# Performance work log

Hardware: AMD Instinct MI355X
Metric: run time of the kernel (lower is better)

## Reference

```python
import jax, jax.numpy as jnp
import numpy as np

K = 5       # kernel_size
UP = 2      # up_factor
EPS = 1e-5  # BatchNorm eps (eval mode)


def _conv(x, w, pad, dil=1):
    return jax.lax.conv_general_dilated(
        x, w, (1, 1), [(pad, pad), (pad, pad)], rhs_dilation=(dil, dil),
        dimension_numbers=('NCHW', 'OIHW', 'NCHW'))


def _bn(x, g, b, m, v):
    inv = g / jnp.sqrt(v + EPS)
    return x * inv[:, None, None] + (b - m * inv)[:, None, None]


def _bilinear(x, oh, ow):
    # torch F.interpolate(mode='bilinear', align_corners=False)
    N, C, H, W = x.shape
    def coords(out_s, in_s):
        s = in_s / out_s
        src = (jnp.arange(out_s, dtype=jnp.float32) + 0.5) * s - 0.5
        src = jnp.clip(src, 0.0, in_s - 1)
        i0 = jnp.floor(src).astype(jnp.int32)
        i1 = jnp.minimum(i0 + 1, in_s - 1)
        return i0, i1, src - i0
    y0, y1, wy = coords(oh, H)
    x0, x1, wx = coords(ow, W)
    g = lambda yi, xi: x[:, :, yi][:, :, :, xi]  # (N,C,oh,ow)
    top = g(y0, x0) * (1 - wx) + g(y0, x1) * wx
    bot = g(y1, x0) * (1 - wx) + g(y1, x1) * wx
    return top * (1 - wy)[:, None] + bot * wy[:, None]


def _unfold(x):
    # F.unfold(k=5, pad=2) reshaped to (N, C, K*K, H, W); channel-major (c, kh, kw)
    p = K // 2
    N, C, H, W = x.shape
    xp = jnp.pad(x, ((0, 0), (0, 0), (p, p), (p, p)))
    patches = [xp[:, :, i:i + H, j:j + W] for i in range(K) for j in range(K)]
    return jnp.stack(patches, axis=2)


def setup_inputs() -> dict:
    key = jax.random.key(0)
    ks = jax.random.split(key, 8)
    N, C, H, W = 2, 256, 48, 48
    Cc = C // 4
    Cout = 256
    d = {}
    d['x'] = jax.random.normal(ks[0], (N, C, H, W), dtype=jnp.float32)
    d['compress_w'] = jax.random.normal(ks[1], (Cc, C, 1, 1), dtype=jnp.float32) * 0.05
    d['g1'] = jnp.ones((Cc,), jnp.float32)
    d['b1'] = jnp.zeros((Cc,), jnp.float32)
    d['m1'] = jax.random.normal(ks[2], (Cc,), dtype=jnp.float32) * 0.1
    d['v1'] = jax.random.uniform(ks[3], (Cc,), minval=0.5, maxval=1.5, dtype=jnp.float32)
    d['ke1_w'] = jax.random.normal(ks[4], (Cc, Cc, 3, 3), dtype=jnp.float32) * 0.05
    d['gk'] = jnp.ones((Cc,), jnp.float32)
    d['bk'] = jnp.zeros((Cc,), jnp.float32)
    d['mk'] = jax.random.normal(ks[5], (Cc,), dtype=jnp.float32) * 0.1
    d['vk'] = jax.random.uniform(ks[6], (Cc,), minval=0.5, maxval=1.5, dtype=jnp.float32)
    d['ke2_w'] = jax.random.normal(ks[7], (UP * UP * K * K, Cc, 3, 3), dtype=jnp.float32) * 0.05
    d['proj_w'] = jax.random.normal(jax.random.fold_in(key, 10), (Cout, C, 1, 1), dtype=jnp.float32) * 0.05
    d['g2'] = jnp.ones((Cout,), jnp.float32)
    d['b2'] = jnp.zeros((Cout,), jnp.float32)
    d['m2'] = jax.random.normal(jax.random.fold_in(key, 11), (Cout,), dtype=jnp.float32) * 0.1
    d['v2'] = jax.random.uniform(jax.random.fold_in(key, 12), (Cout,), minval=0.5, maxval=1.5, dtype=jnp.float32)
    return d


def reference(x, compress_w, g1, b1, m1, v1, ke1_w, gk, bk, mk, vk, ke2_w,
              proj_w, g2, b2, m2, v2):
    N, C, H, W = x.shape
    oh, ow = H * UP, W * UP
    # kernel prediction branch
    comp = jax.nn.relu(_bn(_conv(x, compress_w, 0), g1, b1, m1, v1))
    k1 = jax.nn.relu(_bn(_conv(comp, ke1_w, 2, dil=2), gk, bk, mk, vk))
    kernel = _conv(k1, ke2_w, 1)                               # (N, UP^2*K^2, H, W)
    kernel = jax.nn.softmax(kernel.reshape(N, UP * UP, K * K, H, W), axis=2)
    # content reassembly
    x_up = jnp.repeat(jnp.repeat(x, UP, axis=2), UP, axis=3)
    x_unf = _unfold(x_up)                                      # (N, C, K^2, oh, ow)
    k_up = _bilinear(kernel.reshape(N, UP * UP * K * K, H, W), oh, ow)
    k_up = k_up.reshape(N, UP * UP, K * K, oh, ow)
    out = jnp.einsum('nckhw,nukhw->nuchw', x_unf, k_up)        # (N, UP^2, C, oh, ow)
    # view (N, UP^2*C, oh, ow) then pixel_shuffle(UP)
    out = out.reshape(N, UP * UP * C, oh, ow)
    out = out.reshape(N, C, UP, UP, oh, ow)
    out = out.transpose(0, 1, 4, 2, 5, 3).reshape(N, C, oh * UP, ow * UP)
    out = jax.nn.relu(_bn(_conv(out, proj_w, 0), g2, b2, m2, v2))
    return out
```

## Files before the change

### kernel.cpp

```cpp
#include <hip/hip_runtime.h>

#define EPSB 1e-5f

typedef __attribute__((ext_vector_type(8))) short bf16x8;
typedef __attribute__((ext_vector_type(4))) float f32x4;

__device__ __forceinline__ unsigned short f2b(float f) {
  union { float f; unsigned u; } cv; cv.f = f;
  unsigned r = cv.u + 0x7FFFu + ((cv.u >> 16) & 1u);
  return (unsigned short)(r >> 16);
}

__global__ __launch_bounds__(256) void k_prep(
    const float* __restrict__ pw, const float* __restrict__ cw,
    const float* __restrict__ k1w, const float* __restrict__ k2w,
    const float* __restrict__ g1, const float* __restrict__ b1,
    const float* __restrict__ m1, const float* __restrict__ v1,
    const float* __restrict__ gk, const float* __restrict__ bk,
    const float* __restrict__ mk, const float* __restrict__ vk,
    const float* __restrict__ g2, const float* __restrict__ b2,
    const float* __restrict__ m2, const float* __restrict__ v2,
    unsigned short* __restrict__ pwb, unsigned short* __restrict__ wcb_t,
    unsigned short* __restrict__ wt1, unsigned short* __restrict__ wt2,
    float* __restrict__ sb1, float* __restrict__ sbk, float* __restrict__ sb2,
    float* __restrict__ wsz) {
  int i = blockIdx.x * 256 + threadIdx.x;
  if (i < 333056) wsz[i] = 0.f;
  if (i < 65536) pwb[i] = f2b(pw[i]);
  int j = i - 65536;
  if (j >= 0 && j < 16384) { int ci = j >> 6, co = j & 63; wcb_t[j] = f2b(cw[co * 256 + ci]); }
  int a = i - 81920;
  if (a >= 0 && a < 36864) {
    int co = a / 576, k = a % 576, tap = k >> 6, ci = k & 63;
    wt1[a] = f2b(k1w[co * 576 + ci * 9 + tap]);
  }
  int c2 = i - 118784;
  if (c2 >= 0 && c2 < 73728) {
    int co = c2 / 576, k = c2 % 576, tap = k >> 6, ci = k & 63;
    wt2[c2] = (co < 100) ? f2b(k2w[co * 576 + ci * 9 + tap]) : (unsigned short)0;
  }
  int s = i - 192512;
  if (s >= 0 && s < 64) { float iv = g1[s] / sqrtf(v1[s] + EPSB); sb1[s] = iv; sb1[64 + s] = b1[s] - m1[s] * iv; }
  if (s >= 64 && s < 128) { int c = s - 64; float iv = gk[c] / sqrtf(vk[c] + EPSB); sbk[c] = iv; sbk[64 + c] = bk[c] - mk[c] * iv; }
  if (s >= 128 && s < 384) { int c = s - 128; float iv = g2[c] / sqrtf(v2[c] + EPSB); sb2[c] = iv; sb2[256 + c] = b2[c] - m2[c] * iv; }
}

__global__ __launch_bounds__(256) void k_compress(
    const float* __restrict__ x, const unsigned short* __restrict__ wcb_t,
    const float* __restrict__ sb1, unsigned short* __restrict__ comp_t) {
  __shared__ unsigned short wl[16384];
  int t = threadIdx.x;
  for (int f = t; f < 2048; f += 256)
    *(bf16x8*)&wl[f * 8] = *(const bf16x8*)&wcb_t[f * 8];
  __syncthreads();
  int idx = blockIdx.x * 256 + t;
  int co2 = (idx & 31) * 2;
  int pg = idx >> 5;
  int n = pg / 1152;
  int pix0 = (pg % 1152) * 2;
  const float* xp = x + (size_t)n * 256 * 2304 + pix0;
  float a00 = 0.f, a01 = 0.f, a10 = 0.f, a11 = 0.f;
  for (int ci = 0; ci < 256; ++ci) {
    float2 xv = *(const float2*)(xp + (size_t)ci * 2304);
    unsigned pr = *(const unsigned*)&wl[ci * 64 + co2];
    union { unsigned u; float f; } wa, wb;
    wa.u = pr << 16; wb.u = pr & 0xffff0000u;
    a00 = fmaf(xv.x, wa.f, a00); a01 = fmaf(xv.y, wa.f, a01);
    a10 = fmaf(xv.x, wb.f, a10); a11 = fmaf(xv.y, wb.f, a11);
  }
  float s0 = sb1[co2], s1 = sb1[co2 + 1];
  float c0b = sb1[64 + co2], c1b = sb1[64 + co2 + 1];
  float o00 = fmaxf(fmaf(a00, s0, c0b), 0.f), o01 = fmaxf(fmaf(a01, s0, c0b), 0.f);
  float o10 = fmaxf(fmaf(a10, s1, c1b), 0.f), o11 = fmaxf(fmaf(a11, s1, c1b), 0.f);
  int r = pix0 / 48, c = pix0 % 48;
  unsigned short* ob = comp_t + ((size_t)n * 2704 + (r + 2) * 52 + (c + 2)) * 64 + co2;
  unsigned p0 = (unsigned)f2b(o00) | ((unsigned)f2b(o10) << 16);
  unsigned p1 = (unsigned)f2b(o01) | ((unsigned)f2b(o11) << 16);
  *(unsigned*)&ob[0]  = p0;
  *(unsigned*)&ob[64] = p1;
}

__global__ __launch_bounds__(256) void k_ke1(
    const unsigned short* __restrict__ comp_t, const unsigned short* __restrict__ wt1,
    const float* __restrict__ sbk, unsigned short* __restrict__ k1_t) {
  __shared__ unsigned short sA[16640];
  int t = threadIdx.x;
  int bid = blockIdx.x;
  int n = bid / 48, y = bid % 48;
  const unsigned short* src = comp_t + ((size_t)n * 52 + y) * 52 * 64;
  for (int f = t; f < 2080; f += 256) {
    int g = f >> 3, ci0 = (f & 7) * 8;
    int cc = g % 52, rr = g / 52;
    bf16x8 vv = *(const bf16x8*)&src[(rr * 52 + cc) * 64 + ci0];
    int ba = (((rr * 52 + cc) * 64 + ci0) * 2) ^ ((cc & 7) << 4);
    *(bf16x8*)((char*)sA + ba) = vv;
  }
  __syncthreads();
  int wid = t >> 6, l = t & 63, l15 = l & 15, lg = l >> 4;
  f32x4 acc[3];
  acc[0] = acc[1] = acc[2] = (f32x4){0.f, 0.f, 0.f, 0.f};
  const unsigned short* arow = wt1 + (size_t)(wid * 16 + l15) * 576;
#pragma unroll
  for (int kbi = 0; kbi < 18; ++kbi) {
    int tap = kbi >> 1;
    int ky = tap / 3, kx = tap % 3;
    int ci0 = (kbi & 1) * 32 + lg * 8;
    bf16x8 afr = *(const bf16x8*)&arow[kbi * 32 + lg * 8];
#pragma unroll
    for (int nt = 0; nt < 3; ++nt) {
      int col = nt * 16 + l15 + 2 * kx;
      int ba = (((2 * ky * 52 + col) * 64 + ci0) * 2) ^ ((col & 7) << 4);
      bf16x8 bfr = *(const bf16x8*)((char*)sA + ba);
      acc[nt] = __builtin_amdgcn_mfma_f32_16x16x32_bf16(afr, bfr, acc[nt], 0, 0, 0);
    }
  }
  unsigned short* dst = k1_t + ((size_t)n * 50 + (y + 1)) * 50 * 64;
  int co0 = wid * 16 + lg * 4;
  float s0 = sbk[co0], s1 = sbk[co0 + 1], s2 = sbk[co0 + 2], s3 = sbk[co0 + 3];
  float d0 = sbk[64 + co0], d1 = sbk[64 + co0 + 1], d2 = sbk[64 + co0 + 2], d3 = sbk[64 + co0 + 3];
#pragma unroll
  for (int nt = 0; nt < 3; ++nt) {
    int px = nt * 16 + l15;
    ushort4 pk;
    pk.x = f2b(fmaxf(fmaf(acc[nt][0], s0, d0), 0.f));
    pk.y = f2b(fmaxf(fmaf(acc[nt][1], s1, d1), 0.f));
    pk.z = f2b(fmaxf(fmaf(acc[nt][2], s2, d2), 0.f));
    pk.w = f2b(fmaxf(fmaf(acc[nt][3], s3, d3), 0.f));
    *(ushort4*)&dst[(px + 1) * 64 + co0] = pk;
  }
}

__global__ __launch_bounds__(256) void k_ke2(
    const unsigned short* __restrict__ k1_t, const unsigned short* __restrict__ wt2,
    float* __restrict__ kern_t) {
  __shared__ unsigned short sA[9600];
  int t = threadIdx.x;
  int bid = blockIdx.x;
  int n = bid / 48, y = bid % 48;
  const unsigned short* src = k1_t + ((size_t)n * 50 + y) * 50 * 64;
  for (int f = t; f < 1200; f += 256) {
    int g = f >> 3, ci0 = (f & 7) * 8;
    int cc = g % 50, rr = g / 50;
    bf16x8 vv = *(const bf16x8*)&src[(rr * 50 + cc) * 64 + ci0];
    int ba = (((rr * 50 + cc) * 64 + ci0) * 2) ^ ((cc & 7) << 4);
    *(bf16x8*)((char*)sA + ba) = vv;
  }
  __syncthreads();
  int wid = t >> 6, l = t & 63, l15 = l & 15, lg = l >> 4;
  f32x4 acc[2][3];
#pragma unroll
  for (int mi = 0; mi < 2; ++mi)
#pragma unroll
    for (int nt = 0; nt < 3; ++nt) acc[mi][nt] = (f32x4){0.f, 0.f, 0.f, 0.f};
#pragma unroll
  for (int kbi = 0; kbi < 18; ++kbi) {
    int tap = kbi >> 1;
    int ky = tap / 3, kx = tap % 3;
    int ci0 = (kbi & 1) * 32 + lg * 8;
    bf16x8 afr[2];
#pragma unroll
    for (int mi = 0; mi < 2; ++mi)
      afr[mi] = *(const bf16x8*)&wt2[(size_t)((wid * 2 + mi) * 16 + l15) * 576 + kbi * 32 + lg * 8];
#pragma unroll
    for (int nt = 0; nt < 3; ++nt) {
      int col = nt * 16 + l15 + kx;
      int ba = (((ky * 50 + col) * 64 + ci0) * 2) ^ ((col & 7) << 4);
      bf16x8 bfr = *(const bf16x8*)((char*)sA + ba);
      acc[0][nt] = __builtin_amdgcn_mfma_f32_16x16x32_bf16(afr[0], bfr, acc[0][nt], 0, 0, 0);
      acc[1][nt] = __builtin_amdgcn_mfma_f32_16x16x32_bf16(afr[1], bfr, acc[1][nt], 0, 0, 0);
    }
  }
#pragma unroll
  for (int mi = 0; mi < 2; ++mi) {
    int co0 = (wid * 2 + mi) * 16 + lg * 4;
    if (co0 < 100) {
#pragma unroll
      for (int nt = 0; nt < 3; ++nt) {
        int px = nt * 16 + l15;
        float4 vv = {acc[mi][nt][0], acc[mi][nt][1], acc[mi][nt][2], acc[mi][nt][3]};
        *(float4*)&kern_t[((size_t)n * 2304 + y * 48 + px) * 112 + co0] = vv;
      }
    }
  }
}

__global__ __launch_bounds__(256) void k_w9sm(const float* __restrict__ kern_t,
                                              float* __restrict__ w9) {
  __shared__ float ks[3 * 48 * 116];
  int bid = blockIdx.x;
  int n = bid / 48, k = bid % 48;
  int t = threadIdx.x;
  int rows[3] = {max(k - 1, 0), k, min(k + 1, 47)};
#pragma unroll
  for (int s = 0; s < 3; ++s) {
    const float* src = kern_t + ((size_t)n * 2304 + rows[s] * 48) * 112;
    for (int f = t; f < 1344; f += 256) {
      float4 vv = *(const float4*)&src[f * 4];
      int sx = f / 28, c = (f % 28) * 4;
      *(float4*)&ks[(s * 48 + sx) * 116 + c] = vv;
    }
  }
  __syncthreads();
#pragma unroll
  for (int it = 0; it < 3; ++it) {
    int f = t + it * 256;
    int half = f / 384, rem = f % 384;
    int w2 = rem >> 2, u = rem & 3;
    int y96 = 2 * k + half;
    float syf = fminf(fmaxf(y96 * 0.5f - 0.25f, 0.f), 47.f);
    int y0 = (int)syf; int y1 = min(y0 + 1, 47); float wy = syf - (float)y0;
    int sl0 = (y0 == k) ? 1 : 0;
    int sl1 = (y1 == k) ? 1 : 2;
    float sxf = fminf(fmaxf(w2 * 0.5f - 0.25f, 0.f), 47.f);
    int x0 = (int)sxf; int x1 = min(x0 + 1, 47); float wx = sxf - (float)x0;
    float bl[25];
#pragma unroll
    for (int kk = 0; kk < 25; ++kk) bl[kk] = 0.f;
    float ws4[4] = {(1.f - wx) * (1.f - wy), wx * (1.f - wy), (1.f - wx) * wy, wx * wy};
    int ssy[4] = {sl0, sl0, sl1, sl1};
    int ssx[4] = {x0, x1, x0, x1};
#pragma unroll
    for (int s = 0; s < 4; ++s) {
      const float* p = &ks[(ssy[s] * 48 + ssx[s]) * 116 + u * 25];
      float vv[25], mx = -3.4e38f;
#pragma unroll
      for (int kk = 0; kk < 25; ++kk) { vv[kk] = p[kk]; mx = fmaxf(mx, vv[kk]); }
      float sum = 0.f;
#pragma unroll
      for (int kk = 0; kk < 25; ++kk) { vv[kk] = __expf(vv[kk] - mx); sum += vv[kk]; }
      float rs = ws4[s] / sum;
#pragma unroll
      for (int kk = 0; kk < 25; ++kk) bl[kk] = fmaf(vv[kk], rs, bl[kk]);
    }
#pragma unroll
    for (int kh = 0; kh < 5; ++kh) {
      bool vy = (unsigned)(y96 + kh - 2) < 96u;
#pragma unroll
      for (int kw = 0; kw < 5; ++kw) {
        bool vx = (unsigned)(w2 + kw - 2) < 96u;
        if (!(vy && vx)) bl[kh * 5 + kw] = 0.f;
      }
    }
    int py = y96 & 1, px_ = w2 & 1;
    float cc0[5], cc1[5], cc2[5];
#pragma unroll
    for (int kh = 0; kh < 5; ++kh) {
      cc0[kh] = px_ ? bl[kh * 5 + 0] : bl[kh * 5 + 0] + bl[kh * 5 + 1];
      cc1[kh] = px_ ? bl[kh * 5 + 1] + bl[kh * 5 + 2] : bl[kh * 5 + 2] + bl[kh * 5 + 3];
      cc2[kh] = px_ ? bl[kh * 5 + 3] + bl[kh * 5 + 4] : bl[kh * 5 + 4];
    }
    float* op = w9 + (((size_t)(n * 96 + y96) * 96 + w2) * 4 + u) * 9;
    op[0] = py ? cc0[0] : cc0[0] + cc0[1];
    op[1] = py ? cc1[0] : cc1[0] + cc1[1];
    op[2] = py ? cc2[0] : cc2[0] + cc2[1];
    op[3] = py ? cc0[1] + cc0[2] : cc0[2] + cc0[3];
    op[4] = py ? cc1[1] + cc1[2] : cc1[2] + cc1[3];
    op[5] = py ? cc2[1] + cc2[2] : cc2[2] + cc2[3];
    op[6] = py ? cc0[3] + cc0[4] : cc0[4];
    op[7] = py ? cc1[3] + cc1[4] : cc1[4];
    op[8] = py ? cc2[3] + cc2[4] : cc2[4];
  }
}

__global__ __launch_bounds__(512, 4) void k_reassemble_proj(
    const float* __restrict__ x, const float* __restrict__ w9,
    const unsigned short* __restrict__ pwb, const float* __restrict__ sb2,
    float* __restrict__ out) {
  __shared__ float xls[256 * 35];
  __shared__ float w9s[1152];
  __shared__ float sb2s[512];
  __shared__ unsigned short finT[64 * 256];

  int blk = blockIdx.x;
  int n = blk / 288;
  int r = blk % 288;
  int y48 = r / 6;
  int xt = r % 6;
  int X0 = xt * 32;
  int x480 = xt * 8;
  int t = threadIdx.x;

  sb2s[t] = sb2[t];
  {
    const float* base = w9 + ((size_t)(n * 96 + 2 * y48) * 96 + xt * 16) * 36;
    for (int f = t; f < 1152; f += 512) {
      int half = f / 576, o = f - half * 576;
      w9s[f] = base[(size_t)half * 3456 + o];
    }
  }
  const float* xb = x + (size_t)n * 256 * 2304;
  for (int f = t; f < 8448; f += 512) {
    int c = f / 33, rc = f - c * 33;
    int ry = rc / 11, cx = rc - ry * 11;
    int sy = min(max(y48 + ry - 1, 0), 47);
    int sx = min(max(x480 + cx - 1, 0), 47);
    int slot = (c & 3) * 64 + (c >> 2);
    xls[slot * 35 + rc] = xb[(size_t)c * 2304 + sy * 48 + sx];
  }
  __syncthreads();

  int ci = t & 255, rY = t >> 8;
  int u = ci >> 6, ch = ci & 63;
  int cb = ci >> 3, crr = ci & 7;
  int wid = t >> 6, l = t & 63, l15 = l & 15, lg = l >> 4;
  const unsigned short* a0p = pwb + (size_t)(wid * 2 * 16 + l15) * 256;
  const unsigned short* a1p = a0p + 16 * 256;
  size_t outn = (size_t)n * 256 * 36864;
  int Ybase = 4 * y48;

#pragma unroll
  for (int chunk = 0; chunk < 2; ++chunk) {
    {
      const float* xc0 = &xls[((rY * 2 + 0) * 64 + ch) * 35];
      const float* xc1 = &xls[((rY * 2 + 1) * 64 + ch) * 35];
      float xw0[9], xw1[9];
#pragma unroll
      for (int ry = 0; ry < 3; ++ry)
#pragma unroll
        for (int cx = 0; cx < 3; ++cx) {
          xw0[ry * 3 + cx] = xc0[ry * 11 + cx];
          xw1[ry * 3 + cx] = xc1[ry * 11 + cx];
        }
#pragma unroll
      for (int j = 0; j < 16; ++j) {
        if (j >= 2 && (j & 1) == 0) {
          int nc = (j >> 1) + 2;
#pragma unroll
          for (int ry = 0; ry < 3; ++ry) {
            xw0[ry*3+0]=xw0[ry*3+1]; xw0[ry*3+1]=xw0[ry*3+2]; xw0[ry*3+2]=xc0[ry*11+nc];
            xw1[ry*3+0]=xw1[ry*3+1]; xw1[ry*3+1]=xw1[ry*3+2]; xw1[ry*3+2]=xc1[ry*11+nc];
          }
        }
        const float* wt = &w9s[(chunk * 16 + j) * 36 + u * 9];
        float a0 = 0.f, a1 = 0.f;
#pragma unroll
        for (int k9 = 0; k9 < 9; ++k9) {
          float wv = wt[k9];
          a0 = fmaf(xw0[k9], wv, a0);
          a1 = fmaf(xw1[k9], wv, a1);
        }
        int px0 = rY * 32 + 2 * j, px1 = px0 + 1;
        finT[px0 * 256 + ((cb ^ (px0 & 7)) * 8 + crr)] = f2b(a0);
        finT[px1 * 256 + ((cb ^ (px1 & 7)) * 8 + crr)] = f2b(a1);
      }
    }
    __syncthreads();

    f32x4 acc[2][4];
#pragma unroll
    for (int mi = 0; mi < 2; ++mi)
#pragma unroll
      for (int nt = 0; nt < 4; ++nt) acc[mi][nt] = (f32x4){0.f, 0.f, 0.f, 0.f};
#pragma unroll
    for (int kbi = 0; kbi < 8; ++kbi) {
      bf16x8 afr0 = *(const bf16x8*)&a0p[kbi * 32 + lg * 8];
      bf16x8 afr1 = *(const bf16x8*)&a1p[kbi * 32 + lg * 8];
      int cbk = kbi * 4 + lg;
#pragma unroll
      for (int nt = 0; nt < 4; ++nt) {
        int row = nt * 16 + l15;
        bf16x8 bfr = *(const bf16x8*)&finT[row * 256 + ((cbk ^ (row & 7)) * 8)];
        acc[0][nt] = __builtin_amdgcn_mfma_f32_16x16x32_bf16(afr0, bfr, acc[0][nt], 0, 0, 0);
        acc[1][nt] = __builtin_amdgcn_mfma_f32_16x16x32_bf16(afr1, bfr, acc[1][nt], 0, 0, 0);
      }
    }
#pragma unroll
    for (int mi = 0; mi < 2; ++mi) {
      int mt = wid * 2 + mi;
#pragma unroll
      for (int r4 = 0; r4 < 4; ++r4) {
        int o = mt * 16 + lg * 4 + r4;
        float sc = sb2s[o], bi = sb2s[256 + o];
#pragma unroll
        for (int nt = 0; nt < 4; ++nt) {
          int px = nt * 16 + l15;
          int Yl = chunk * 2 + (px >> 5), Xl = px & 31;
          float val = fmaxf(fmaf(acc[mi][nt][r4], sc, bi), 0.f);
          out[outn + (size_t)o * 36864 + (size_t)(Ybase + Yl) * 192 + X0 + Xl] = val;
        }
      }
    }
    __syncthreads();
  }
}

extern "C" void kernel_launch(void* const* d_in, const int* in_sizes, int n_in,
                              void* d_out, int out_size, void* d_ws, size_t ws_size,
                              hipStream_t stream) {
  const float* x   = (const float*)d_in[0];
  const float* cw  = (const float*)d_in[1];
  const float* g1  = (const float*)d_in[2];
  const float* b1  = (const float*)d_in[3];
  const float* m1  = (const float*)d_in[4];
  const float* v1  = (const float*)d_in[5];
  const float* k1w = (const float*)d_in[6];
  const float* gk  = (const float*)d_in[7];
  const float* bk  = (const float*)d_in[8];
  const float* mk  = (const float*)d_in[9];
  const float* vk  = (const float*)d_in[10];
  const float* k2w = (const float*)d_in[11];
  const float* pw  = (const float*)d_in[12];
  const float* g2  = (const float*)d_in[13];
  const float* b2  = (const float*)d_in[14];
  const float* m2  = (const float*)d_in[15];
  const float* v2  = (const float*)d_in[16];
  float* out = (float*)d_out;
  float* ws  = (float*)d_ws;

  unsigned short* comp_t = (unsigned short*)ws;
  unsigned short* k1_t   = (unsigned short*)(ws + 173056);
  float* kern_t = ws + 333056;
  float* w9     = ws + 849152;
  unsigned short* pwb   = (unsigned short*)(ws + 1512704);
  unsigned short* wcb_t = (unsigned short*)(ws + 1545472);
  unsigned short* wt1   = (unsigned short*)(ws + 1553664);
  unsigned short* wt2   = (unsigned short*)(ws + 1572096);
  float* sb1 = ws + 1608960;
  float* sbk = ws + 1609088;
  float* sb2 = ws + 1609216;

  k_prep<<<1302, 256, 0, stream>>>(pw, cw, k1w, k2w, g1, b1, m1, v1,
                                   gk, bk, mk, vk, g2, b2, m2, v2,
                                   pwb, wcb_t, wt1, wt2, sb1, sbk, sb2, ws);
  k_compress<<<288, 256, 0, stream>>>(x, wcb_t, sb1, comp_t);
  k_ke1<<<96, 256, 0, stream>>>(comp_t, wt1, sbk, k1_t);
  k_ke2<<<96, 256, 0, stream>>>(k1_t, wt2, kern_t);
  k_w9sm<<<96, 256, 0, stream>>>(kern_t, w9);
  k_reassemble_proj<<<576, 512, 0, stream>>>(x, w9, pwb, sb2, out);
}
```

Before: 202.0 us.

## Double-buffer reassembly tile and overlap with projection MFMA per output row

Restructures the fused reassemble+projection kernel into four per-row stages, with a double-buffered bf16 tile in shared memory. Reassembly for the next row is computed while the current row's MFMA projection and output stores run, which removes one barrier per stage. The w9 weights are padded from 9 to 12 floats so they can be read as float4 vectors. The cost is a larger w9 buffer with shifted workspace offsets, more register pressure from the sliding 6-wide windows, and smaller MFMA groups per stage.

```diff
diff --git a/kernel.cpp b/kernel.cpp
--- a/kernel.cpp
+++ b/kernel.cpp
@@ -249,7 +249,7 @@
       cc1[kh] = px_ ? bl[kh * 5 + 1] + bl[kh * 5 + 2] : bl[kh * 5 + 2] + bl[kh * 5 + 3];
       cc2[kh] = px_ ? bl[kh * 5 + 3] + bl[kh * 5 + 4] : bl[kh * 5 + 4];
     }
-    float* op = w9 + (((size_t)(n * 96 + y96) * 96 + w2) * 4 + u) * 9;
+    float* op = w9 + (((size_t)(n * 96 + y96) * 96 + w2) * 4 + u) * 12;
     op[0] = py ? cc0[0] : cc0[0] + cc0[1];
     op[1] = py ? cc1[0] : cc1[0] + cc1[1];
     op[2] = py ? cc2[0] : cc2[0] + cc2[1];
@@ -262,14 +262,60 @@
   }
 }
 
+__device__ __forceinline__ void compute_vals(
+    const float* __restrict__ xls, const float* __restrict__ w9s,
+    int c, int ch, int u, int jb, float* __restrict__ v0, float* __restrict__ v1) {
+  int p = c & 1;
+  const float* xc0 = &xls[((2 * p + 0) * 64 + ch) * 35];
+  const float* xc1 = &xls[((2 * p + 1) * 64 + ch) * 35];
+  int cbase = jb >> 1;
+  float w60[3][6], w61[3][6];
+#pragma unroll
+  for (int ry = 0; ry < 3; ++ry)
+#pragma unroll
+    for (int cc = 0; cc < 6; ++cc) {
+      w60[ry][cc] = xc0[ry * 11 + cbase + cc];
+      w61[ry][cc] = xc1[ry * 11 + cbase + cc];
+    }
+  const float* wrow = &w9s[((c >> 1) * 16 + jb) * 48 + u * 12];
+#pragma unroll
+  for (int jj = 0; jj < 8; ++jj) {
+    const float* wt = wrow + jj * 48;
+    float4 wa = *(const float4*)wt;
+    float4 wb = *(const float4*)(wt + 4);
+    float w8 = wt[8];
+    int cs = jj >> 1;
+    float a0 = w60[0][cs] * wa.x;
+    a0 = fmaf(w60[0][cs + 1], wa.y, a0);
+    a0 = fmaf(w60[0][cs + 2], wa.z, a0);
+    a0 = fmaf(w60[1][cs],     wa.w, a0);
+    a0 = fmaf(w60[1][cs + 1], wb.x, a0);
+    a0 = fmaf(w60[1][cs + 2], wb.y, a0);
+    a0 = fmaf(w60[2][cs],     wb.z, a0);
+    a0 = fmaf(w60[2][cs + 1], wb.w, a0);
+    a0 = fmaf(w60[2][cs + 2], w8,   a0);
+    float a1 = w61[0][cs] * wa.x;
+    a1 = fmaf(w61[0][cs + 1], wa.y, a1);
+    a1 = fmaf(w61[0][cs + 2], wa.z, a1);
+    a1 = fmaf(w61[1][cs],     wa.w, a1);
+    a1 = fmaf(w61[1][cs + 1], wb.x, a1);
+    a1 = fmaf(w61[1][cs + 2], wb.y, a1);
+    a1 = fmaf(w61[2][cs],     wb.z, a1);
+    a1 = fmaf(w61[2][cs + 1], wb.w, a1);
+    a1 = fmaf(w61[2][cs + 2], w8,   a1);
+    v0[jj] = a0;
+    v1[jj] = a1;
+  }
+}
+
 __global__ __launch_bounds__(512, 4) void k_reassemble_proj(
     const float* __restrict__ x, const float* __restrict__ w9,
     const unsigned short* __restrict__ pwb, const float* __restrict__ sb2,
     float* __restrict__ out) {
   __shared__ float xls[256 * 35];
-  __shared__ float w9s[1152];
+  __shared__ float w9s[1536];
   __shared__ float sb2s[512];
-  __shared__ unsigned short finT[64 * 256];
+  __shared__ unsigned short finT[2][32 * 256];
 
   int blk = blockIdx.x;
   int n = blk / 288;
@@ -282,10 +328,10 @@
 
   sb2s[t] = sb2[t];
   {
-    const float* base = w9 + ((size_t)(n * 96 + 2 * y48) * 96 + xt * 16) * 36;
-    for (int f = t; f < 1152; f += 512) {
-      int half = f / 576, o = f - half * 576;
-      w9s[f] = base[(size_t)half * 3456 + o];
+    const float* wbase = w9 + ((size_t)(n * 96 + 2 * y48) * 96 + xt * 16) * 48;
+    for (int f = t; f < 1536; f += 512) {
+      int half = f / 768, o = f - half * 768;
+      w9s[f] = wbase[(size_t)half * 4608 + o];
     }
   }
   const float* xb = x + (size_t)n * 256 * 2304;
@@ -299,88 +345,72 @@
   }
   __syncthreads();
 
-  int ci = t & 255, rY = t >> 8;
+  int ci = t & 255, half = t >> 8;
   int u = ci >> 6, ch = ci & 63;
   int cb = ci >> 3, crr = ci & 7;
+  int jb = half * 8;
   int wid = t >> 6, l = t & 63, l15 = l & 15, lg = l >> 4;
   const unsigned short* a0p = pwb + (size_t)(wid * 2 * 16 + l15) * 256;
   const unsigned short* a1p = a0p + 16 * 256;
   size_t outn = (size_t)n * 256 * 36864;
   int Ybase = 4 * y48;
 
-#pragma unroll
-  for (int chunk = 0; chunk < 2; ++chunk) {
-    {
-      const float* xc0 = &xls[((rY * 2 + 0) * 64 + ch) * 35];
-      const float* xc1 = &xls[((rY * 2 + 1) * 64 + ch) * 35];
-      float xw0[9], xw1[9];
-#pragma unroll
-      for (int ry = 0; ry < 3; ++ry)
-#pragma unroll
-        for (int cx = 0; cx < 3; ++cx) {
-          xw0[ry * 3 + cx] = xc0[ry * 11 + cx];
-          xw1[ry * 3 + cx] = xc1[ry * 11 + cx];
-        }
-#pragma unroll
-      for (int j = 0; j < 16; ++j) {
-        if (j >= 2 && (j & 1) == 0) {
-          int nc = (j >> 1) + 2;
-#pragma unroll
-          for (int ry = 0; ry < 3; ++ry) {
-            xw0[ry*3+0]=xw0[ry*3+1]; xw0[ry*3+1]=xw0[ry*3+2]; xw0[ry*3+2]=xc0[ry*11+nc];
-            xw1[ry*3+0]=xw1[ry*3+1]; xw1[ry*3+1]=xw1[ry*3+2]; xw1[ry*3+2]=xc1[ry*11+nc];
-          }
-        }
-        const float* wt = &w9s[(chunk * 16 + j) * 36 + u * 9];
-        float a0 = 0.f, a1 = 0.f;
-#pragma unroll
-        for (int k9 = 0; k9 < 9; ++k9) {
-          float wv = wt[k9];
-          a0 = fmaf(xw0[k9], wv, a0);
-          a1 = fmaf(xw1[k9], wv, a1);
-        }
-        int px0 = rY * 32 + 2 * j, px1 = px0 + 1;
-        finT[px0 * 256 + ((cb ^ (px0 & 7)) * 8 + crr)] = f2b(a0);
-        finT[px1 * 256 + ((cb ^ (px1 & 7)) * 8 + crr)] = f2b(a1);
-      }
-    }
-    __syncthreads();
-
-    f32x4 acc[2][4];
+  float v0[8], v1[8];
+  compute_vals(xls, w9s, 0, ch, u, jb, v0, v1);
+#pragma unroll
+  for (int jj = 0; jj < 8; ++jj) {
+    int px0 = 2 * (jb + jj), px1 = px0 + 1;
+    finT[0][px0 * 256 + ((cb ^ (px0 & 7)) * 8 + crr)] = f2b(v0[jj]);
+    finT[0][px1 * 256 + ((cb ^ (px1 & 7)) * 8 + crr)] = f2b(v1[jj]);
+  }
+  __syncthreads();
+
+#pragma unroll
+  for (int c = 0; c < 4; ++c) {
+    f32x4 acc[2][2];
 #pragma unroll
     for (int mi = 0; mi < 2; ++mi)
 #pragma unroll
-      for (int nt = 0; nt < 4; ++nt) acc[mi][nt] = (f32x4){0.f, 0.f, 0.f, 0.f};
+      for (int nt = 0; nt < 2; ++nt) acc[mi][nt] = (f32x4){0.f, 0.f, 0.f, 0.f};
 #pragma unroll
     for (int kbi = 0; kbi < 8; ++kbi) {
       bf16x8 afr0 = *(const bf16x8*)&a0p[kbi * 32 + lg * 8];
       bf16x8 afr1 = *(const bf16x8*)&a1p[kbi * 32 + lg * 8];
       int cbk = kbi * 4 + lg;
 #pragma unroll
-      for (int nt = 0; nt < 4; ++nt) {
+      for (int nt = 0; nt < 2; ++nt) {
         int row = nt * 16 + l15;
-        bf16x8 bfr = *(const bf16x8*)&finT[row * 256 + ((cbk ^ (row & 7)) * 8)];
+        bf16x8 bfr = *(const bf16x8*)&finT[c & 1][row * 256 + ((cbk ^ (row & 7)) * 8)];
         acc[0][nt] = __builtin_amdgcn_mfma_f32_16x16x32_bf16(afr0, bfr, acc[0][nt], 0, 0, 0);
         acc[1][nt] = __builtin_amdgcn_mfma_f32_16x16x32_bf16(afr1, bfr, acc[1][nt], 0, 0, 0);
       }
     }
-#pragma unroll
-    for (int mi = 0; mi < 2; ++mi) {
-      int mt = wid * 2 + mi;
-#pragma unroll
-      for (int r4 = 0; r4 < 4; ++r4) {
-        int o = mt * 16 + lg * 4 + r4;
-        float sc = sb2s[o], bi = sb2s[256 + o];
-#pragma unroll
-        for (int nt = 0; nt < 4; ++nt) {
-          int px = nt * 16 + l15;
-          int Yl = chunk * 2 + (px >> 5), Xl = px & 31;
-          float val = fmaxf(fmaf(acc[mi][nt][r4], sc, bi), 0.f);
-          out[outn + (size_t)o * 36864 + (size_t)(Ybase + Yl) * 192 + X0 + Xl] = val;
+    if (c < 3) compute_vals(xls, w9s, c + 1, ch, u, jb, v0, v1);
+    {
+      float* orow = out + outn + (size_t)(Ybase + c) * 192 + X0;
+#pragma unroll
+      for (int mi = 0; mi < 2; ++mi) {
+#pragma unroll
+        for (int r4 = 0; r4 < 4; ++r4) {
+          int o = (wid * 2 + mi) * 16 + lg * 4 + r4;
+          float sc = sb2s[o], bi = sb2s[256 + o];
+#pragma unroll
+          for (int nt = 0; nt < 2; ++nt) {
+            float val = fmaxf(fmaf(acc[mi][nt][r4], sc, bi), 0.f);
+            orow[(size_t)o * 36864 + nt * 16 + l15] = val;
+          }
         }
       }
     }
-    __syncthreads();
+    if (c < 3) {
+#pragma unroll
+      for (int jj = 0; jj < 8; ++jj) {
+        int px0 = 2 * (jb + jj), px1 = px0 + 1;
+        finT[(c + 1) & 1][px0 * 256 + ((cb ^ (px0 & 7)) * 8 + crr)] = f2b(v0[jj]);
+        finT[(c + 1) & 1][px1 * 256 + ((cb ^ (px1 & 7)) * 8 + crr)] = f2b(v1[jj]);
+      }
+      __syncthreads();
+    }
   }
 }
 
@@ -411,13 +441,13 @@
   unsigned short* k1_t   = (unsigned short*)(ws + 173056);
   float* kern_t = ws + 333056;
   float* w9     = ws + 849152;
-  unsigned short* pwb   = (unsigned short*)(ws + 1512704);
-  unsigned short* wcb_t = (unsigned short*)(ws + 1545472);
-  unsigned short* wt1   = (unsigned short*)(ws + 1553664);
-  unsigned short* wt2   = (unsigned short*)(ws + 1572096);
-  float* sb1 = ws + 1608960;
-  float* sbk = ws + 1609088;
-  float* sb2 = ws + 1609216;
+  unsigned short* pwb   = (unsigned short*)(ws + 1733888);
+  unsigned short* wcb_t = (unsigned short*)(ws + 1766656);
+  unsigned short* wt1   = (unsigned short*)(ws + 1774848);
+  unsigned short* wt2   = (unsigned short*)(ws + 1793280);
+  float* sb1 = ws + 1830144;
+  float* sbk = ws + 1830272;
+  float* sb2 = ws + 1830400;
 
   k_prep<<<1302, 256, 0, stream>>>(pw, cw, k1w, k2w, g1, b1, m1, v1,
                                    gk, bk, mk, vk, g2, b2, m2, v2,
```

Result: slower. 230.5 us (+14.1%).
